# Performance work log

Measured on AMD Instinct MI355X. Metric: run time of the kernel, lower is better.

## Reference

```python
import jax, jax.numpy as jnp
import numpy as np

N, E, R, D, DEPTH = 50000, 800000, 1000, 128, 2


def setup_inputs() -> dict:
    key = jax.random.key(0)
    ks = jax.random.split(key, 6)
    features = jax.random.normal(ks[0], (N, D), jnp.float32)
    rel_emb = jax.random.normal(ks[1], (R, D), jnp.float32)
    # adj coalesced by row (torch coalesce sorts indices; values stay aligned)
    src = jnp.sort(jax.random.randint(ks[2], (E,), 0, N))
    dst = jax.random.randint(ks[3], (E,), 0, N)
    adj = jnp.stack([src, dst]).astype(jnp.int64)
    # one relation per triple: row index = triple id, col = relation id
    r_index = jnp.stack([jnp.arange(E), jax.random.randint(ks[4], (E,), 0, R)]).astype(jnp.int64)
    r_val = jax.random.uniform(ks[5], (E,), jnp.float32)
    attn_kernels = jax.random.normal(jax.random.fold_in(key, 7), (DEPTH, D), jnp.float32) * 0.1
    return {"features": features, "rel_emb": rel_emb, "adj": adj, "r_index": r_index,
            "r_val": r_val, "triple_size": E, "rel_size": R, "node_size": N,
            "attn_kernels": attn_kernels}


def _layer(features, rel_emb, adj, r_index, r_val, triple_size, node_size, attn_k):
    row = adj[0]
    neighs = features[adj[1]]                                   # [E, D] gather
    # sparse.mm(tri_rel, rel_emb): sum_j r_val * rel_emb[col] per triple row
    tri_rel = jax.ops.segment_sum(r_val[:, None] * rel_emb[r_index[1]],
                                  r_index[0], num_segments=triple_size)  # [E, D]
    nrm = jnp.linalg.norm(tri_rel, axis=1, keepdims=True)
    tri_rel = tri_rel / jnp.maximum(nrm, 1e-12)                 # F.normalize(p=2)
    # Householder-style reflection
    neighs = neighs - 2.0 * jnp.sum(neighs * tri_rel, axis=1, keepdims=True) * tri_rel
    att = tri_rel @ attn_k                                      # [E]
    # sparse row-wise softmax over edges grouped by destination row
    m = jax.ops.segment_max(att, row, num_segments=node_size)
    e = jnp.exp(att - m[row])
    s = jax.ops.segment_sum(e, row, num_segments=node_size)
    att = e / s[row]
    new_features = jax.ops.segment_sum(neighs * att[:, None], row,
                                       num_segments=node_size)  # [N, D] scatter
    return jnp.tanh(new_features)


def reference(features, rel_emb, adj, r_index, r_val, triple_size, rel_size, node_size, attn_kernels):
    features = jnp.tanh(features)
    outputs = [features]
    for l in range(attn_kernels.shape[0]):
        features = _layer(features, rel_emb, adj, r_index, r_val,
                          triple_size, node_size, attn_kernels[l])
        outputs.append(features)
    return jnp.concatenate(outputs, axis=-1)                    # [N, D*(depth+1)]
```

## Files before the change

### kernel.cpp

```cpp
#include <hip/hip_runtime.h>
#include <hip/hip_bf16.h>
#include <math.h>

#define N_NODES   50000
#define N_EDGES   800000
#define N_REL     1000
#define DIM       128
#define DEPTH_L   2
#define OUT_STRIDE (DIM * (DEPTH_L + 1))

typedef _Float16 h2 __attribute__((ext_vector_type(2)));

#if defined(__has_builtin)
#if __has_builtin(__builtin_amdgcn_fdot2)
#define FDOT2(a, b, c) __builtin_amdgcn_fdot2((a), (b), (c), false)
#endif
#endif
#ifndef FDOT2
#define FDOT2(a, b, c) ((c) + (float)(a).x * (float)(b).x + (float)(a).y * (float)(b).y)
#endif

__device__ __forceinline__ float fast_tanh(float x) {
    float cx = fminf(fmaxf(x, -15.f), 15.f);
    float e = __expf(2.f * cx);
    return (e - 1.f) * __frcp_rn(e + 1.f);
}

__global__ __launch_bounds__(64) void prep_rel_kernel(
    const float* __restrict__ rel_emb,
    const float* __restrict__ attn_k,
    _Float16* __restrict__ rhat,
    float* __restrict__ att_rel)
{
    int r = blockIdx.x;
    int lane = threadIdx.x;
    if (r == N_REL) {
        rhat[(size_t)r * DIM + lane]      = (_Float16)0.f;
        rhat[(size_t)r * DIM + lane + 64] = (_Float16)0.f;
        if (lane < DEPTH_L) att_rel[lane * (N_REL + 1) + N_REL] = 0.f;
        return;
    }
    float v0 = rel_emb[r * DIM + lane];
    float v1 = rel_emb[r * DIM + lane + 64];
    float ss = v0 * v0 + v1 * v1;
    #pragma unroll
    for (int o = 32; o >= 1; o >>= 1) ss += __shfl_xor(ss, o);
    float inv = 1.0f / fmaxf(sqrtf(ss), 1e-12f);
    float t0 = v0 * inv, t1 = v1 * inv;
    rhat[(size_t)r * DIM + lane]      = (_Float16)t0;
    rhat[(size_t)r * DIM + lane + 64] = (_Float16)t1;
    #pragma unroll
    for (int l = 0; l < DEPTH_L; ++l) {
        float d = t0 * attn_k[l * DIM + lane] + t1 * attn_k[l * DIM + lane + 64];
        #pragma unroll
        for (int o = 32; o >= 1; o >>= 1) d += __shfl_xor(d, o);
        if (lane == 0) att_rel[l * (N_REL + 1) + r] = d;
    }
}

__global__ __launch_bounds__(256) void rowptr_kernel(
    const int* __restrict__ src, int* __restrict__ rp)
{
    int n = blockIdx.x * blockDim.x + threadIdx.x;
    if (n > N_NODES) return;
    int lo = 0, hi = N_EDGES;
    while (lo < hi) {
        int mid = (lo + hi) >> 1;
        if (src[mid] < n) lo = mid + 1; else hi = mid;
    }
    rp[n] = lo;
}

__global__ __launch_bounds__(128) void weights_tanh_kernel(
    const float* __restrict__ feat, float* __restrict__ out,
    _Float16* __restrict__ fs0,
    const int* __restrict__ dst, const int* __restrict__ relid,
    const float* __restrict__ rval, const int* __restrict__ rp,
    const float* __restrict__ att_rel,
    uint2* __restrict__ einfo2)
{
    int wid  = threadIdx.x >> 6;
    int lane = threadIdx.x & 63;
    int node = blockIdx.x * 2 + wid;
    if (node >= N_NODES) return;

    float2 v = *reinterpret_cast<const float2*>(feat + (size_t)node * DIM + 2 * lane);
    float y0 = fast_tanh(v.x), y1 = fast_tanh(v.y);
    *reinterpret_cast<float2*>(out + (size_t)node * OUT_STRIDE + 2 * lane)
        = make_float2(y0, y1);
    h2 pr; pr.x = (_Float16)y0; pr.y = (_Float16)y1;
    *reinterpret_cast<h2*>(fs0 + (size_t)node * DIM + 2 * lane) = pr;

    int start = rp[node], end = rp[node + 1];
    if (start >= end) return;
    const float* ar0 = att_rel;
    const float* ar1 = att_rel + (N_REL + 1);

    float m0 = -INFINITY, s0 = 0.f, m1 = -INFINITY, s1 = 0.f;
    for (int e = start + lane; e < end; e += 64) {
        int r = (rval[e] == 0.f) ? N_REL : relid[e];
        float l0 = ar0[r], l1 = ar1[r];
        if (l0 > m0) { s0 = s0 * __expf(m0 - l0) + 1.f; m0 = l0; }
        else         { s0 += __expf(l0 - m0); }
        if (l1 > m1) { s1 = s1 * __expf(m1 - l1) + 1.f; m1 = l1; }
        else         { s1 += __expf(l1 - m1); }
    }
    #pragma unroll
    for (int o = 32; o >= 1; o >>= 1) {
        float ma = __shfl_xor(m0, o), sa = __shfl_xor(s0, o);
        float mn = fmaxf(m0, ma);
        s0 = (mn == -INFINITY) ? 0.f : s0 * __expf(m0 - mn) + sa * __expf(ma - mn);
        m0 = mn;
        float mb = __shfl_xor(m1, o), sb = __shfl_xor(s1, o);
        float mo = fmaxf(m1, mb);
        s1 = (mo == -INFINITY) ? 0.f : s1 * __expf(m1 - mo) + sb * __expf(mb - mo);
        m1 = mo;
    }
    float i0 = 1.0f / s0, i1 = 1.0f / s1;
    for (int e = start + lane; e < end; e += 64) {
        int r = (rval[e] == 0.f) ? N_REL : relid[e];
        float w0 = __expf(ar0[r] - m0) * i0;
        float w1 = __expf(ar1[r] - m1) * i1;
        h2 wp; wp.x = (_Float16)w0; wp.y = (_Float16)w1;
        einfo2[e] = make_uint2((unsigned)dst[e] | ((unsigned)r << 16),
                               __builtin_bit_cast(unsigned, wp));
    }
}

template<int L>
__global__ __launch_bounds__(128) void layer_fused_kernel(
    const _Float16* __restrict__ fs_in,
    float* __restrict__ fout,
    _Float16* __restrict__ fs_out,
    const uint2* __restrict__ einfo2,
    const int* __restrict__ rp,
    const _Float16* __restrict__ rhat)
{
    int wid  = threadIdx.x >> 6;
    int lane = threadIdx.x & 63;
    int node = blockIdx.x * 2 + wid;
    if (node >= N_NODES) return;
    int start = rp[node], end = rp[node + 1];
    int g = lane >> 3;
    int q = lane & 7;

    const char* fbase = (const char*)fs_in + 32 * q;
    const char* tbase = (const char*)rhat  + 32 * q;
    int g0 = (lane >> 3) & 1, g1 = (lane >> 4) & 1, g2 = (lane >> 5) & 1;

    h2 a2[8];
    #pragma unroll
    for (int i = 0; i < 8; ++i) { a2[i].x = (_Float16)0.f; a2[i].y = (_Float16)0.f; }

    for (int e0 = start; e0 < end; e0 += 16) {
        int eL = end - 1;
        int ea = e0 + g;
        int ca = (ea < eL) ? ea : eL;
        uint2 ia = einfo2[ca];
        int eb = e0 + 8 + g;
        int cb = (eb < eL) ? eb : eL;
        uint2 ib = einfo2[cb];

        unsigned dnA = ia.x & 0xffffu, rlA = ia.x >> 16;
        unsigned dnB = ib.x & 0xffffu, rlB = ib.x >> 16;
        const uint4* hpA = reinterpret_cast<const uint4*>(fbase + (size_t)dnA * 256);
        const uint4* tpA = reinterpret_cast<const uint4*>(tbase + (size_t)rlA * 256);
        const uint4* hpB = reinterpret_cast<const uint4*>(fbase + (size_t)dnB * 256);
        const uint4* tpB = reinterpret_cast<const uint4*>(tbase + (size_t)rlB * 256);
        uint4 hA0 = hpA[0], hA1 = hpA[1];
        uint4 tA0 = tpA[0], tA1 = tpA[1];
        uint4 hB0 = hpB[0], hB1 = hpB[1];
        uint4 tB0 = tpB[0], tB1 = tpB[1];

        h2 wpA = __builtin_bit_cast(h2, ia.y);
        h2 wpB = __builtin_bit_cast(h2, ib.y);
        _Float16 wA = (ea < end) ? ((L == 0) ? wpA.x : wpA.y) : (_Float16)0.f;
        _Float16 wB = (eb < end) ? ((L == 0) ? wpB.x : wpB.y) : (_Float16)0.f;

        __builtin_amdgcn_sched_barrier(0);

        {
            h2 hh[8], tt[8];
            hh[0] = __builtin_bit_cast(h2, hA0.x); hh[1] = __builtin_bit_cast(h2, hA0.y);
            hh[2] = __builtin_bit_cast(h2, hA0.z); hh[3] = __builtin_bit_cast(h2, hA0.w);
            hh[4] = __builtin_bit_cast(h2, hA1.x); hh[5] = __builtin_bit_cast(h2, hA1.y);
            hh[6] = __builtin_bit_cast(h2, hA1.z); hh[7] = __builtin_bit_cast(h2, hA1.w);
            tt[0] = __builtin_bit_cast(h2, tA0.x); tt[1] = __builtin_bit_cast(h2, tA0.y);
            tt[2] = __builtin_bit_cast(h2, tA0.z); tt[3] = __builtin_bit_cast(h2, tA0.w);
            tt[4] = __builtin_bit_cast(h2, tA1.x); tt[5] = __builtin_bit_cast(h2, tA1.y);
            tt[6] = __builtin_bit_cast(h2, tA1.z); tt[7] = __builtin_bit_cast(h2, tA1.w);
            float d0 = 0.f, d1 = 0.f;
            #pragma unroll
            for (int p = 0; p < 8; p += 2) {
                d0 = FDOT2(hh[p],     tt[p],     d0);
                d1 = FDOT2(hh[p + 1], tt[p + 1], d1);
            }
            float d = d0 + d1;
            d += __shfl_xor(d, 1);
            d += __shfl_xor(d, 2);
            d += __shfl_xor(d, 4);
            float cf = -2.f * (float)wA * d;
            _Float16 cfh = (_Float16)cf;
            h2 wv; wv.x = wA;  wv.y = wA;
            h2 cv; cv.x = cfh; cv.y = cfh;
            #pragma unroll
            for (int p = 0; p < 8; ++p) {
                a2[p] = hh[p] * wv + a2[p];
                a2[p] = tt[p] * cv + a2[p];
            }
        }

        {
            h2 hh[8], tt[8];
            hh[0] = __builtin_bit_cast(h2, hB0.x); hh[1] = __builtin_bit_cast(h2, hB0.y);
            hh[2] = __builtin_bit_cast(h2, hB0.z); hh[3] = __builtin_bit_cast(h2, hB0.w);
            hh[4] = __builtin_bit_cast(h2, hB1.x); hh[5] = __builtin_bit_cast(h2, hB1.y);
            hh[6] = __builtin_bit_cast(h2, hB1.z); hh[7] = __builtin_bit_cast(h2, hB1.w);
            tt[0] = __builtin_bit_cast(h2, tB0.x); tt[1] = __builtin_bit_cast(h2, tB0.y);
            tt[2] = __builtin_bit_cast(h2, tB0.z); tt[3] = __builtin_bit_cast(h2, tB0.w);
            tt[4] = __builtin_bit_cast(h2, tB1.x); tt[5] = __builtin_bit_cast(h2, tB1.y);
            tt[6] = __builtin_bit_cast(h2, tB1.z); tt[7] = __builtin_bit_cast(h2, tB1.w);
            float d0 = 0.f, d1 = 0.f;
            #pragma unroll
            for (int p = 0; p < 8; p += 2) {
                d0 = FDOT2(hh[p],     tt[p],     d0);
                d1 = FDOT2(hh[p + 1], tt[p + 1], d1);
            }
            float d = d0 + d1;
            d += __shfl_xor(d, 1);
            d += __shfl_xor(d, 2);
            d += __shfl_xor(d, 4);
            float cf = -2.f * (float)wB * d;
            _Float16 cfh = (_Float16)cf;
            h2 wv; wv.x = wB;  wv.y = wB;
            h2 cv; cv.x = cfh; cv.y = cfh;
            #pragma unroll
            for (int p = 0; p < 8; ++p) {
                a2[p] = hh[p] * wv + a2[p];
                a2[p] = tt[p] * cv + a2[p];
            }
        }
    }

    h2 b1[4];
    #pragma unroll
    for (int k = 0; k < 4; ++k) {
        h2 keep = g0 ? a2[2*k + 1] : a2[2*k];
        h2 send = g0 ? a2[2*k] : a2[2*k + 1];
        unsigned su = __shfl_xor(__builtin_bit_cast(unsigned, send), 8);
        b1[k] = keep + __builtin_bit_cast(h2, su);
    }
    h2 b2[2];
    #pragma unroll
    for (int m = 0; m < 2; ++m) {
        h2 keep = g1 ? b1[2*m + 1] : b1[2*m];
        h2 send = g1 ? b1[2*m] : b1[2*m + 1];
        unsigned su = __shfl_xor(__builtin_bit_cast(unsigned, send), 16);
        b2[m] = keep + __builtin_bit_cast(h2, su);
    }
    h2 c;
    {
        h2 keep = g2 ? b2[1] : b2[0];
        h2 send = g2 ? b2[0] : b2[1];
        unsigned su = __shfl_xor(__builtin_bit_cast(unsigned, send), 32);
        c = keep + __builtin_bit_cast(h2, su);
    }

    float y0 = fast_tanh((float)c.x), y1 = fast_tanh((float)c.y);
    int dimo = 16 * q + 2 * g;
    *reinterpret_cast<float2*>(fout + (size_t)node * OUT_STRIDE + dimo)
        = make_float2(y0, y1);
    if (L == 0) {
        h2 pr; pr.x = (_Float16)y0; pr.y = (_Float16)y1;
        *reinterpret_cast<h2*>(fs_out + (size_t)node * DIM + dimo) = pr;
    }
}

extern "C" void kernel_launch(void* const* d_in, const int* in_sizes, int n_in,
                              void* d_out, int out_size, void* d_ws, size_t ws_size,
                              hipStream_t stream)
{
    const float* features = (const float*)d_in[0];
    const float* rel_emb  = (const float*)d_in[1];
    const int*   adj      = (const int*)d_in[2];
    const int*   r_index  = (const int*)d_in[3];
    const float* r_val    = (const float*)d_in[4];
    const float* attn_k   = (const float*)d_in[8];
    float* out = (float*)d_out;

    const int* src   = adj;
    const int* dst   = adj + N_EDGES;
    const int* relid = r_index + N_EDGES;

    char* base = (char*)d_ws;
    _Float16* rhat    = (_Float16*)base;
    float*    att_rel = (float*)(base + 256256);
    int*      rp      = (int*)(base + 264264);
    uint2*    einfo2  = (uint2*)(base + 464272);
    _Float16* fs0     = (_Float16*)(base + 464272 + (size_t)N_EDGES * 8);
    _Float16* fs1     = fs0 + (size_t)N_NODES * DIM;

    prep_rel_kernel<<<N_REL + 1, 64, 0, stream>>>(rel_emb, attn_k, rhat, att_rel);
    rowptr_kernel<<<(N_NODES + 1 + 255) / 256, 256, 0, stream>>>(src, rp);
    weights_tanh_kernel<<<(N_NODES + 1) / 2, 128, 0, stream>>>(
        features, out, fs0, dst, relid, r_val, rp, att_rel, einfo2);

    layer_fused_kernel<0><<<(N_NODES + 1) / 2, 128, 0, stream>>>(
        fs0, out + 1 * DIM, fs1, einfo2, rp, rhat);
    layer_fused_kernel<1><<<(N_NODES + 1) / 2, 128, 0, stream>>>(
        fs1, out + 2 * DIM, fs0, einfo2, rp, rhat);
}
```

Baseline: 125.2 us.

## Precompute exp of relation logits and build softmax sums with edge-parallel segmented scan

Softmax weights are no longer computed per node with an online max/sum. Instead exp(logit) is precomputed per relation, and each edge stores the fp16 exp values. Per-node sums come from an edge-parallel warp segmented scan plus atomics, and division by the sum moves into the layer kernels. The feature tanh becomes its own fully parallel kernel. This drops max subtraction, so large logits could overflow fp16 or fp32, and it adds atomics and an extra launch.

```diff
diff --git a/kernel.cpp b/kernel.cpp
--- a/kernel.cpp
+++ b/kernel.cpp
@@ -30,14 +30,14 @@
     const float* __restrict__ rel_emb,
     const float* __restrict__ attn_k,
     _Float16* __restrict__ rhat,
-    float* __restrict__ att_rel)
+    float* __restrict__ er0, float* __restrict__ er1)
 {
     int r = blockIdx.x;
     int lane = threadIdx.x;
     if (r == N_REL) {
         rhat[(size_t)r * DIM + lane]      = (_Float16)0.f;
         rhat[(size_t)r * DIM + lane + 64] = (_Float16)0.f;
-        if (lane < DEPTH_L) att_rel[lane * (N_REL + 1) + N_REL] = 0.f;
+        if (lane == 0) { er0[N_REL] = 1.f; er1[N_REL] = 1.f; }
         return;
     }
     float v0 = rel_emb[r * DIM + lane];
@@ -54,12 +54,15 @@
         float d = t0 * attn_k[l * DIM + lane] + t1 * attn_k[l * DIM + lane + 64];
         #pragma unroll
         for (int o = 32; o >= 1; o >>= 1) d += __shfl_xor(d, o);
-        if (lane == 0) att_rel[l * (N_REL + 1) + r] = d;
+        if (lane == 0) {
+            if (l == 0) er0[r] = __expf(d); else er1[r] = __expf(d);
+        }
     }
 }
 
 __global__ __launch_bounds__(256) void rowptr_kernel(
-    const int* __restrict__ src, int* __restrict__ rp)
+    const int* __restrict__ src, int* __restrict__ rp,
+    float* __restrict__ s0, float* __restrict__ s1)
 {
     int n = blockIdx.x * blockDim.x + threadIdx.x;
     if (n > N_NODES) return;
@@ -69,61 +72,60 @@
         if (src[mid] < n) lo = mid + 1; else hi = mid;
     }
     rp[n] = lo;
-}
-
-__global__ __launch_bounds__(128) void weights_tanh_kernel(
+    if (n < N_NODES) { s0[n] = 0.f; s1[n] = 0.f; }
+}
+
+__global__ __launch_bounds__(256) void tanh0_kernel(
     const float* __restrict__ feat, float* __restrict__ out,
-    _Float16* __restrict__ fs0,
-    const int* __restrict__ dst, const int* __restrict__ relid,
-    const float* __restrict__ rval, const int* __restrict__ rp,
-    const float* __restrict__ att_rel,
+    _Float16* __restrict__ fs0)
+{
+    int i = blockIdx.x * blockDim.x + threadIdx.x;
+    if (i >= N_NODES * 32) return;
+    int n = i >> 5;
+    int j = i & 31;
+    float4 v = reinterpret_cast<const float4*>(feat + (size_t)n * DIM)[j];
+    float4 o;
+    o.x = fast_tanh(v.x); o.y = fast_tanh(v.y);
+    o.z = fast_tanh(v.z); o.w = fast_tanh(v.w);
+    reinterpret_cast<float4*>(out + (size_t)n * OUT_STRIDE)[j] = o;
+    h2 p0; p0.x = (_Float16)o.x; p0.y = (_Float16)o.y;
+    h2 p1; p1.x = (_Float16)o.z; p1.y = (_Float16)o.w;
+    uint2 u;
+    u.x = __builtin_bit_cast(unsigned, p0);
+    u.y = __builtin_bit_cast(unsigned, p1);
+    reinterpret_cast<uint2*>(fs0 + (size_t)n * DIM)[j] = u;
+}
+
+__global__ __launch_bounds__(256) void sum_einfo_kernel(
+    const int* __restrict__ src, const int* __restrict__ dst,
+    const int* __restrict__ relid, const float* __restrict__ rval,
+    const float* __restrict__ er0, const float* __restrict__ er1,
+    float* __restrict__ s0, float* __restrict__ s1,
     uint2* __restrict__ einfo2)
 {
-    int wid  = threadIdx.x >> 6;
+    int e = blockIdx.x * 256 + threadIdx.x;
+    if (e >= N_EDGES) return;
     int lane = threadIdx.x & 63;
-    int node = blockIdx.x * 2 + wid;
-    if (node >= N_NODES) return;
-
-    float2 v = *reinterpret_cast<const float2*>(feat + (size_t)node * DIM + 2 * lane);
-    float y0 = fast_tanh(v.x), y1 = fast_tanh(v.y);
-    *reinterpret_cast<float2*>(out + (size_t)node * OUT_STRIDE + 2 * lane)
-        = make_float2(y0, y1);
-    h2 pr; pr.x = (_Float16)y0; pr.y = (_Float16)y1;
-    *reinterpret_cast<h2*>(fs0 + (size_t)node * DIM + 2 * lane) = pr;
-
-    int start = rp[node], end = rp[node + 1];
-    if (start >= end) return;
-    const float* ar0 = att_rel;
-    const float* ar1 = att_rel + (N_REL + 1);
-
-    float m0 = -INFINITY, s0 = 0.f, m1 = -INFINITY, s1 = 0.f;
-    for (int e = start + lane; e < end; e += 64) {
-        int r = (rval[e] == 0.f) ? N_REL : relid[e];
-        float l0 = ar0[r], l1 = ar1[r];
-        if (l0 > m0) { s0 = s0 * __expf(m0 - l0) + 1.f; m0 = l0; }
-        else         { s0 += __expf(l0 - m0); }
-        if (l1 > m1) { s1 = s1 * __expf(m1 - l1) + 1.f; m1 = l1; }
-        else         { s1 += __expf(l1 - m1); }
-    }
-    #pragma unroll
-    for (int o = 32; o >= 1; o >>= 1) {
-        float ma = __shfl_xor(m0, o), sa = __shfl_xor(s0, o);
-        float mn = fmaxf(m0, ma);
-        s0 = (mn == -INFINITY) ? 0.f : s0 * __expf(m0 - mn) + sa * __expf(ma - mn);
-        m0 = mn;
-        float mb = __shfl_xor(m1, o), sb = __shfl_xor(s1, o);
-        float mo = fmaxf(m1, mb);
-        s1 = (mo == -INFINITY) ? 0.f : s1 * __expf(m1 - mo) + sb * __expf(mb - mo);
-        m1 = mo;
-    }
-    float i0 = 1.0f / s0, i1 = 1.0f / s1;
-    for (int e = start + lane; e < end; e += 64) {
-        int r = (rval[e] == 0.f) ? N_REL : relid[e];
-        float w0 = __expf(ar0[r] - m0) * i0;
-        float w1 = __expf(ar1[r] - m1) * i1;
-        h2 wp; wp.x = (_Float16)w0; wp.y = (_Float16)w1;
-        einfo2[e] = make_uint2((unsigned)dst[e] | ((unsigned)r << 16),
-                               __builtin_bit_cast(unsigned, wp));
+    int sn = src[e];
+    int r = (rval[e] == 0.f) ? N_REL : relid[e];
+    float x0 = er0[r], x1 = er1[r];
+
+    h2 ep; ep.x = (_Float16)x0; ep.y = (_Float16)x1;
+    einfo2[e] = make_uint2((unsigned)dst[e] | ((unsigned)r << 16),
+                           __builtin_bit_cast(unsigned, ep));
+
+    #pragma unroll
+    for (int off = 1; off < 64; off <<= 1) {
+        float y0 = __shfl_up(x0, off);
+        float y1 = __shfl_up(x1, off);
+        int   sp = __shfl_up(sn, off);
+        if (lane >= off && sp == sn) { x0 += y0; x1 += y1; }
+    }
+    int snext = __shfl_down(sn, 1);
+    bool lastlane = (lane == 63) || (e == N_EDGES - 1) || (snext != sn);
+    if (lastlane) {
+        atomicAdd(&s0[sn], x0);
+        atomicAdd(&s1[sn], x1);
     }
 }
 
@@ -134,6 +136,7 @@
     _Float16* __restrict__ fs_out,
     const uint2* __restrict__ einfo2,
     const int* __restrict__ rp,
+    const float* __restrict__ s_l,
     const _Float16* __restrict__ rhat)
 {
     int wid  = threadIdx.x >> 6;
@@ -143,6 +146,8 @@
     int start = rp[node], end = rp[node + 1];
     int g = lane >> 3;
     int q = lane & 7;
+
+    float inv_s = 1.0f / s_l[node];
 
     const char* fbase = (const char*)fs_in + 32 * q;
     const char* tbase = (const char*)rhat  + 32 * q;
@@ -172,10 +177,12 @@
         uint4 hB0 = hpB[0], hB1 = hpB[1];
         uint4 tB0 = tpB[0], tB1 = tpB[1];
 
-        h2 wpA = __builtin_bit_cast(h2, ia.y);
-        h2 wpB = __builtin_bit_cast(h2, ib.y);
-        _Float16 wA = (ea < end) ? ((L == 0) ? wpA.x : wpA.y) : (_Float16)0.f;
-        _Float16 wB = (eb < end) ? ((L == 0) ? wpB.x : wpB.y) : (_Float16)0.f;
+        h2 epA = __builtin_bit_cast(h2, ia.y);
+        h2 epB = __builtin_bit_cast(h2, ib.y);
+        float erA = (float)((L == 0) ? epA.x : epA.y);
+        float erB = (float)((L == 0) ? epB.x : epB.y);
+        float wAf = (ea < end) ? erA * inv_s : 0.f;
+        float wBf = (eb < end) ? erB * inv_s : 0.f;
 
         __builtin_amdgcn_sched_barrier(0);
 
@@ -199,9 +206,10 @@
             d += __shfl_xor(d, 1);
             d += __shfl_xor(d, 2);
             d += __shfl_xor(d, 4);
-            float cf = -2.f * (float)wA * d;
+            float cf = -2.f * wAf * d;
+            _Float16 wh  = (_Float16)wAf;
             _Float16 cfh = (_Float16)cf;
-            h2 wv; wv.x = wA;  wv.y = wA;
+            h2 wv; wv.x = wh;  wv.y = wh;
             h2 cv; cv.x = cfh; cv.y = cfh;
             #pragma unroll
             for (int p = 0; p < 8; ++p) {
@@ -230,9 +238,10 @@
             d += __shfl_xor(d, 1);
             d += __shfl_xor(d, 2);
             d += __shfl_xor(d, 4);
-            float cf = -2.f * (float)wB * d;
+            float cf = -2.f * wBf * d;
+            _Float16 wh  = (_Float16)wBf;
             _Float16 cfh = (_Float16)cf;
-            h2 wv; wv.x = wB;  wv.y = wB;
+            h2 wv; wv.x = wh;  wv.y = wh;
             h2 cv; cv.x = cfh; cv.y = cfh;
             #pragma unroll
             for (int p = 0; p < 8; ++p) {
@@ -293,20 +302,24 @@
     const int* relid = r_index + N_EDGES;
 
     char* base = (char*)d_ws;
-    _Float16* rhat    = (_Float16*)base;
-    float*    att_rel = (float*)(base + 256256);
-    int*      rp      = (int*)(base + 264264);
-    uint2*    einfo2  = (uint2*)(base + 464272);
-    _Float16* fs0     = (_Float16*)(base + 464272 + (size_t)N_EDGES * 8);
-    _Float16* fs1     = fs0 + (size_t)N_NODES * DIM;
-
-    prep_rel_kernel<<<N_REL + 1, 64, 0, stream>>>(rel_emb, attn_k, rhat, att_rel);
-    rowptr_kernel<<<(N_NODES + 1 + 255) / 256, 256, 0, stream>>>(src, rp);
-    weights_tanh_kernel<<<(N_NODES + 1) / 2, 128, 0, stream>>>(
-        features, out, fs0, dst, relid, r_val, rp, att_rel, einfo2);
+    _Float16* rhat = (_Float16*)base;
+    float*    er0  = (float*)(base + 256256);
+    float*    er1  = (float*)(base + 260264);
+    int*      rp   = (int*)(base + 264272);
+    float*    s0   = (float*)(base + 464288);
+    float*    s1   = (float*)(base + 664288);
+    uint2*    einfo2 = (uint2*)(base + 864288);
+    _Float16* fs0  = (_Float16*)(base + 864288 + (size_t)N_EDGES * 8);
+    _Float16* fs1  = fs0 + (size_t)N_NODES * DIM;
+
+    prep_rel_kernel<<<N_REL + 1, 64, 0, stream>>>(rel_emb, attn_k, rhat, er0, er1);
+    rowptr_kernel<<<(N_NODES + 1 + 255) / 256, 256, 0, stream>>>(src, rp, s0, s1);
+    tanh0_kernel<<<(N_NODES * 32 + 255) / 256, 256, 0, stream>>>(features, out, fs0);
+    sum_einfo_kernel<<<(N_EDGES + 255) / 256, 256, 0, stream>>>(
+        src, dst, relid, r_val, er0, er1, s0, s1, einfo2);
 
     layer_fused_kernel<0><<<(N_NODES + 1) / 2, 128, 0, stream>>>(
-        fs0, out + 1 * DIM, fs1, einfo2, rp, rhat);
+        fs0, out + 1 * DIM, fs1, einfo2, rp, s0, rhat);
     layer_fused_kernel<1><<<(N_NODES + 1) / 2, 128, 0, stream>>>(
-        fs1, out + 2 * DIM, fs0, einfo2, rp, rhat);
-}
+        fs1, out + 2 * DIM, fs0, einfo2, rp, s1, rhat);
+}
```

New measurement: 114.1 us. -8.9%, faster.
